# Optimization experiments

Measured on AMD Instinct MI355X. Metric: run time of the kernel, lower is better.

## Reference

```python
import jax, jax.numpy as jnp
import numpy as np

B = 131072      # batch
G = 8           # number of groups
GS = 8          # features per group (n_features = G*GS = 64)
K = 8           # n_basis
O = 16          # kan_out_dim
TOT = G * O     # 128, GroupKANLayer output dim
R = 10          # n_rules
FIN = 20        # fuzzy_in_dim = max(2*n_rules, 8)
EPS_BN = 1e-5


def setup_inputs() -> dict:
    key = jax.random.key(0)
    ks = jax.random.split(key, 8)
    x = jax.random.normal(ks[0], (B, G * GS), dtype=jnp.float32)
    # per-group GaussianRBF params (one shared RBF per group, applied to each feature)
    rbf_centres = jnp.tile(jnp.linspace(-3.0, 3.0, K, dtype=jnp.float32)[None, :], (G, 1))
    rbf_log_widths = jnp.zeros((G, K), dtype=jnp.float32)
    rbf_weights = jax.random.normal(ks[1], (G, K), dtype=jnp.float32) * 0.1
    rbf_linear_w = jnp.ones((G,), dtype=jnp.float32)
    # group projections: kaiming normal fan_in (relu gain sqrt(2))
    proj_W = jax.random.normal(ks[2], (G, O, GS), dtype=jnp.float32) * np.sqrt(2.0 / GS)
    proj_b = jnp.zeros((G, O), dtype=jnp.float32)
    bn1_gamma = jnp.ones((TOT,), dtype=jnp.float32)
    bn1_beta = jnp.zeros((TOT,), dtype=jnp.float32)
    # fuzzy_proj linear (xavier uniform) TOT -> FIN
    a = np.sqrt(6.0 / (TOT + FIN))
    fp_W = jax.random.uniform(ks[3], (FIN, TOT), dtype=jnp.float32, minval=-a, maxval=a)
    fp_b = jnp.zeros((FIN,), dtype=jnp.float32)
    bn2_gamma = jnp.ones((FIN,), dtype=jnp.float32)
    bn2_beta = jnp.zeros((FIN,), dtype=jnp.float32)
    # IT2 fuzzy layer params
    fz_centres = jax.random.uniform(ks[4], (R, FIN), dtype=jnp.float32, minval=-1.0, maxval=1.0)
    fz_log_su = jnp.full((R, FIN), -0.7, dtype=jnp.float32)
    fz_log_sl = jnp.full((R, FIN), -1.2, dtype=jnp.float32)
    # sparse rule head
    head_W = jax.random.normal(ks[5], (1, R), dtype=jnp.float32) * 0.05
    head_b = jnp.zeros((1,), dtype=jnp.float32)
    return {
        'x': x, 'rbf_centres': rbf_centres, 'rbf_log_widths': rbf_log_widths,
        'rbf_weights': rbf_weights, 'rbf_linear_w': rbf_linear_w,
        'proj_W': proj_W, 'proj_b': proj_b,
        'bn1_gamma': bn1_gamma, 'bn1_beta': bn1_beta,
        'fp_W': fp_W, 'fp_b': fp_b, 'bn2_gamma': bn2_gamma, 'bn2_beta': bn2_beta,
        'fz_centres': fz_centres, 'fz_log_su': fz_log_su, 'fz_log_sl': fz_log_sl,
        'head_W': head_W, 'head_b': head_b,
    }


def _batchnorm(h, gamma, beta):
    # training-mode BatchNorm1d: normalize with batch mean / biased variance
    mu = h.mean(axis=0)
    var = h.var(axis=0)
    return (h - mu) * jax.lax.rsqrt(var + EPS_BN) * gamma + beta


def _forward(x, rbf_centres, rbf_log_widths, rbf_weights, rbf_linear_w,
             proj_W, proj_b, bn1_gamma, bn1_beta, fp_W, fp_b,
             bn2_gamma, bn2_beta, fz_centres, fz_log_su, fz_log_sl,
             head_W, head_b):
    b = x.shape[0]
    xg = x.reshape(b, G, GS)                               # groups are contiguous index slices
    sigma = jnp.exp(rbf_log_widths) + 1e-6                 # [G,K]
    # Gaussian RBF over all groups/features at once: [B,G,GS,K]
    rbf = jnp.exp(-0.5 * ((xg[..., None] - rbf_centres[:, None, :]) / sigma[:, None, :]) ** 2)
    act = rbf_linear_w[None, :, None] * xg + jnp.einsum('bgfk,gk->bgf', rbf, rbf_weights)
    proj = jnp.einsum('bgf,gof->bgo', act, proj_W) + proj_b  # grouped linear, [B,G,O]
    h = _batchnorm(proj.reshape(b, TOT), bn1_gamma, bn1_beta)
    # fuzzy_proj: Linear -> BN -> GELU (torch default GELU = exact erf form)
    z = _batchnorm(h @ fp_W.T + fp_b, bn2_gamma, bn2_beta)
    z = jax.nn.gelu(z, approximate=False)                    # [B,FIN]
    # IT2 fuzzy memberships
    su = jnp.exp(fz_log_su) + 1e-6                           # [R,FIN]
    sl = jnp.minimum(jnp.exp(fz_log_sl) + 1e-6, su * 0.9)
    diff = z[:, None, :] - fz_centres[None]                  # [B,R,FIN]
    upper = jnp.exp(-0.5 * (diff / su[None]) ** 2).mean(-1)  # [B,R]
    lower = jnp.exp(-0.5 * (diff / sl[None]) ** 2).mean(-1)
    firing = 0.5 * (upper + lower)
    return firing @ head_W.T + head_b                        # [B,1]


def reference(x, rbf_centres, rbf_log_widths, rbf_weights, rbf_linear_w,
              proj_W, proj_b, bn1_gamma, bn1_beta, fp_W, fp_b,
              bn2_gamma, bn2_beta, fz_centres, fz_log_su, fz_log_sl,
              head_W, head_b):
    return _forward(x, rbf_centres, rbf_log_widths, rbf_weights, rbf_linear_w,
                    proj_W, proj_b, bn1_gamma, bn1_beta, fp_W, fp_b,
                    bn2_gamma, bn2_beta, fz_centres, fz_log_su, fz_log_sl,
                    head_W, head_b)
```

## Files before the change

### kernel.cpp

```cpp
#include <hip/hip_runtime.h>
#include <math.h>

#define B_N 131072
#define R_N 10
#define FIN_N 20

#define WS_STAT1 0
#define ST1_SZ   (64 * 352)
#define WS_MT    22528
#define WS_C     23808
#define WS_STAT2 23828
#define WS_NH    26388
#define WS_Z     26816

__global__ __launch_bounds__(256) void k_act_moments(
    const float* __restrict__ x, const float* __restrict__ cen,
    const float* __restrict__ lw, const float* __restrict__ rw,
    const float* __restrict__ linw, float* __restrict__ stat1)
{
    __shared__ float sAcc[4][8][44];

    const int t = threadIdx.x;
    const int g = t & 7;
    const int rl = t >> 3;

    float c_[8], nh_[8], w_[8];
#pragma unroll
    for (int k = 0; k < 8; ++k) {
        c_[k] = cen[g * 8 + k];
        float s = expf(lw[g * 8 + k]) + 1e-6f;
        nh_[k] = -0.5f / (s * s);
        w_[k] = rw[g * 8 + k];
    }
    const float lin = linw[g];

    float sumA[8], P[36];
#pragma unroll
    for (int f = 0; f < 8; ++f) sumA[f] = 0.0f;
#pragma unroll
    for (int i = 0; i < 36; ++i) P[i] = 0.0f;

    for (int row = blockIdx.x * 32 + rl; row < B_N; row += gridDim.x * 32) {
        const float* xr = x + (size_t)row * 64 + g * 8;
        float4 v0 = *(const float4*)(xr);
        float4 v1 = *(const float4*)(xr + 4);
        float xv[8] = {v0.x, v0.y, v0.z, v0.w, v1.x, v1.y, v1.z, v1.w};
        float act[8];
#pragma unroll
        for (int f = 0; f < 8; ++f) {
            float v = xv[f];
            float a = lin * v;
#pragma unroll
            for (int k = 0; k < 8; ++k) {
                float d = v - c_[k];
                a += w_[k] * __expf(d * d * nh_[k]);
            }
            act[f] = a;
        }
        int idx = 0;
#pragma unroll
        for (int f = 0; f < 8; ++f) {
            sumA[f] += act[f];
#pragma unroll
            for (int f2 = 0; f2 <= f; ++f2) { P[idx] += act[f] * act[f2]; ++idx; }
        }
    }

#pragma unroll
    for (int off = 32; off >= 8; off >>= 1) {
#pragma unroll
        for (int f = 0; f < 8; ++f) sumA[f] += __shfl_down(sumA[f], off, 64);
#pragma unroll
        for (int i = 0; i < 36; ++i) P[i] += __shfl_down(P[i], off, 64);
    }
    const int wave = t >> 6, lane = t & 63;
    if (lane < 8) {
        float* dst = &sAcc[wave][lane][0];
#pragma unroll
        for (int f = 0; f < 8; ++f) dst[f] = sumA[f];
#pragma unroll
        for (int i = 0; i < 36; ++i) dst[8 + i] = P[i];
    }
    __syncthreads();
    for (int i = t; i < 352; i += 256) {
        int gg = i / 44, v = i % 44;
        float s = sAcc[0][gg][v] + sAcc[1][gg][v] + sAcc[2][gg][v] + sAcc[3][gg][v];
        atomicAdd(&stat1[(blockIdx.x & 63) * 352 + i], s);
    }
}

__global__ __launch_bounds__(256) void k_build(
    const float* __restrict__ stat1, const float* __restrict__ fpW,
    const float* __restrict__ fpb, const float* __restrict__ g1,
    const float* __restrict__ b1, const float* __restrict__ Wp,
    const float* __restrict__ pb, const float* __restrict__ lsu,
    const float* __restrict__ lsl,
    float* __restrict__ Mt, float* __restrict__ Cc, float* __restrict__ nh,
    float* __restrict__ stat2)
{
    __shared__ float Am[8][8];
    __shared__ float Sg[8][36];
    __shared__ float a_[128], bb_[128];
    const int t = threadIdx.x;

    for (int i = t; i < 352; i += 256) {
        float s = 0.0f;
        for (int st = 0; st < 64; ++st) s += stat1[st * 352 + i];
        float m = s * (1.0f / B_N);
        int g = i / 44, v = i % 44;
        if (v < 8) Am[g][v] = m; else Sg[g][v - 8] = m;
    }
    __syncthreads();

    if (t < 128) {
        const int g = t >> 4;
        float wv[8];
#pragma unroll
        for (int f = 0; f < 8; ++f) wv[f] = Wp[t * 8 + f];
        float dot = 0.0f;
#pragma unroll
        for (int f = 0; f < 8; ++f) dot += wv[f] * Am[g][f];
        const float pbv = pb[t];
        const float mu = pbv + dot;
        float e2 = pbv * pbv + 2.0f * pbv * dot;
        int idx = 0;
#pragma unroll
        for (int f = 0; f < 8; ++f)
#pragma unroll
            for (int f2 = 0; f2 <= f; ++f2) {
                float c2 = (f2 == f) ? 1.0f : 2.0f;
                e2 += c2 * wv[f] * wv[f2] * Sg[g][idx]; ++idx;
            }
        const float var = e2 - mu * mu;
        const float a = g1[t] * rsqrtf(var + 1e-5f);
        a_[t] = a;
        bb_[t] = b1[t] - mu * a;
    }
    __syncthreads();

    for (int i = t; i < 1280; i += 256) {
        int gf = i / 20, j = i % 20;
        int g = gf >> 3, f = gf & 7;
        float m = 0.0f;
        for (int o = 0; o < 16; ++o) {
            int c = g * 16 + o;
            m += fpW[j * 128 + c] * a_[c] * Wp[c * 8 + f];
        }
        Mt[i] = m;
    }
    if (t < 20) {
        float cj = fpb[t];
        for (int c = 0; c < 128; ++c)
            cj += fpW[t * 128 + c] * (a_[c] * pb[c] + bb_[c]);
        Cc[t] = cj;
    }
    for (int i = t; i < 200; i += 256) {
        float su = expf(lsu[i]) + 1e-6f;
        float sl = fminf(expf(lsl[i]) + 1e-6f, 0.9f * su);
        nh[i] = -0.5f / (su * su);
        nh[200 + i] = -0.5f / (sl * sl);
    }
    for (int i = t; i < 2560; i += 256) stat2[i] = 0.0f;
}

__device__ __forceinline__ void zpre_row(
    const float* __restrict__ xr,
    const float4* __restrict__ sRbf,
    const float* __restrict__ sLin,
    const float* __restrict__ sMt,
    const float* __restrict__ sC,
    float zp[20])
{
#pragma unroll
    for (int j = 0; j < 20; ++j) zp[j] = sC[j];
#pragma unroll 1
    for (int g = 0; g < 8; ++g) {
        float4 v0 = *(const float4*)(xr + g * 8);
        float4 v1 = *(const float4*)(xr + g * 8 + 4);
        float xv[8] = {v0.x, v0.y, v0.z, v0.w, v1.x, v1.y, v1.z, v1.w};
        float act[8];
        float lin = sLin[g];
#pragma unroll
        for (int f = 0; f < 8; ++f) act[f] = lin * xv[f];
#pragma unroll 1
        for (int k = 0; k < 8; ++k) {
            float4 p = sRbf[g * 8 + k];
#pragma unroll
            for (int f = 0; f < 8; ++f) {
                float d = xv[f] - p.x;
                act[f] += p.y * __expf(d * d * p.z);
            }
        }
#pragma unroll 1
        for (int f = 0; f < 8; ++f) {
            float a = act[f];
            const float4* m4 = (const float4*)(sMt + (g * 8 + f) * 20);
            float4 ma = m4[0], mb = m4[1], mc = m4[2], md = m4[3], me = m4[4];
            zp[0] += a * ma.x; zp[1] += a * ma.y; zp[2] += a * ma.z; zp[3] += a * ma.w;
            zp[4] += a * mb.x; zp[5] += a * mb.y; zp[6] += a * mb.z; zp[7] += a * mb.w;
            zp[8] += a * mc.x; zp[9] += a * mc.y; zp[10] += a * mc.z; zp[11] += a * mc.w;
            zp[12] += a * md.x; zp[13] += a * md.y; zp[14] += a * md.z; zp[15] += a * md.w;
            zp[16] += a * me.x; zp[17] += a * me.y; zp[18] += a * me.z; zp[19] += a * me.w;
        }
    }
}

__device__ __forceinline__ void load_rbf_lds(
    const float* cen, const float* lw, const float* rw, const float* linw,
    const float* Mt, const float* Cc,
    float4* sRbf, float* sLin, float* sMt, float* sC, int t)
{
    if (t < 64) {
        float s = expf(lw[t]) + 1e-6f;
        sRbf[t] = make_float4(cen[t], rw[t], -0.5f / (s * s), 0.0f);
    }
    if (t < 8)  sLin[t] = linw[t];
    if (t < 20) sC[t] = Cc[t];
    for (int i = t; i < 1280; i += 256) sMt[i] = Mt[i];
}

__global__ __launch_bounds__(256) void k_zpre_stats(
    const float* __restrict__ x, const float* __restrict__ cen,
    const float* __restrict__ lw, const float* __restrict__ rw,
    const float* __restrict__ linw, const float* __restrict__ Mt,
    const float* __restrict__ Cc, float* __restrict__ zout,
    float* __restrict__ stat2, int store)
{
    __shared__ __align__(16) float4 sRbf[64];
    __shared__ float sLin[8], sC[20];
    __shared__ __align__(16) float sMt[1280];
    __shared__ float sRed[4][8][40];

    const int t = threadIdx.x;
    load_rbf_lds(cen, lw, rw, linw, Mt, Cc, sRbf, sLin, sMt, sC, t);
    __syncthreads();

    const int row = blockIdx.x * 256 + t;
    float zp[20];
    zpre_row(x + (size_t)row * 64, sRbf, sLin, sMt, sC, zp);

    if (store) {
#pragma unroll
        for (int j = 0; j < 20; ++j) zout[(size_t)j * B_N + row] = zp[j];
    }

    float s_[20], q_[20];
#pragma unroll
    for (int j = 0; j < 20; ++j) { s_[j] = zp[j]; q_[j] = zp[j] * zp[j]; }
#pragma unroll
    for (int off = 32; off >= 8; off >>= 1) {
#pragma unroll
        for (int j = 0; j < 20; ++j) {
            s_[j] += __shfl_down(s_[j], off, 64);
            q_[j] += __shfl_down(q_[j], off, 64);
        }
    }
    const int wave = t >> 6, lane = t & 63;
    if (lane < 8) {
#pragma unroll
        for (int j = 0; j < 20; ++j) {
            sRed[wave][lane][j] = s_[j];
            sRed[wave][lane][20 + j] = q_[j];
        }
    }
    __syncthreads();
    if (t < 40) {
        float v = 0.0f;
#pragma unroll
        for (int w = 0; w < 4; ++w)
#pragma unroll
            for (int l = 0; l < 8; ++l) v += sRed[w][l][t];
        atomicAdd(&stat2[(blockIdx.x & 63) * 40 + t], v);
    }
}

__device__ __forceinline__ float gelu_exact(float v) {
    return 0.5f * v * (1.0f + erff(v * 0.70710678118654752440f));
}

__device__ __forceinline__ float fuzzy_head(
    const float z[20], const float4* sFz, const float* sHW, float hb)
{
    float acc = hb;
#pragma unroll 1
    for (int r = 0; r < 10; ++r) {
        float u = 0.0f, l = 0.0f;
#pragma unroll
        for (int j = 0; j < 20; ++j) {
            float4 p = sFz[r * 20 + j];
            float d = z[j] - p.x;
            float dd = d * d;
            u += __expf(dd * p.y);
            l += __expf(dd * p.z);
        }
        acc += sHW[r] * 0.025f * (u + l);
    }
    return acc;
}

__device__ __forceinline__ void bn2_inline(
    const float* stat2, const float* g2, const float* b2,
    float* sT, float* sSc, float* sSh, int t)
{
    if (t < 40) {
        float s = 0.0f;
        for (int st = 0; st < 64; ++st) s += stat2[st * 40 + t];
        sT[t] = s;
    }
    __syncthreads();
    if (t < 20) {
        float mu = sT[t] * (1.0f / B_N);
        float var = sT[20 + t] * (1.0f / B_N) - mu * mu;
        float sc = g2[t] * rsqrtf(var + 1e-5f);
        sSc[t] = sc;
        sSh[t] = b2[t] - mu * sc;
    }
}

__global__ __launch_bounds__(256) void k_out_load(
    const float* __restrict__ zin, const float* __restrict__ stat2,
    const float* __restrict__ g2, const float* __restrict__ b2,
    const float* __restrict__ nh, const float* __restrict__ fzc,
    const float* __restrict__ hW, const float* __restrict__ hb,
    float* __restrict__ out)
{
    __shared__ float sT[40], sSc[20], sSh[20], sHW[10];
    __shared__ __align__(16) float4 sFz[200];
    const int t = threadIdx.x;
    if (t < 10) sHW[t] = hW[t];
    for (int i = t; i < 200; i += 256)
        sFz[i] = make_float4(fzc[i], nh[i], nh[200 + i], 0.0f);
    bn2_inline(stat2, g2, b2, sT, sSc, sSh, t);
    __syncthreads();

    const int row = blockIdx.x * 256 + t;
    float z[20];
#pragma unroll
    for (int j = 0; j < 20; ++j) {
        float zp = zin[(size_t)j * B_N + row];
        z[j] = gelu_exact(sSc[j] * zp + sSh[j]);
    }
    out[row] = fuzzy_head(z, sFz, sHW, hb[0]);
}

__global__ __launch_bounds__(256) void k_out_rec(
    const float* __restrict__ x, const float* __restrict__ cen,
    const float* __restrict__ lw, const float* __restrict__ rw,
    const float* __restrict__ linw, const float* __restrict__ Mt,
    const float* __restrict__ Cc, const float* __restrict__ stat2,
    const float* __restrict__ g2, const float* __restrict__ b2,
    const float* __restrict__ nh, const float* __restrict__ fzc,
    const float* __restrict__ hW, const float* __restrict__ hb,
    float* __restrict__ out)
{
    __shared__ __align__(16) float4 sRbf[64];
    __shared__ float sLin[8], sC[20];
    __shared__ __align__(16) float sMt[1280];
    __shared__ float sT[40], sSc[20], sSh[20], sHW[10];
    __shared__ __align__(16) float4 sFz[200];

    const int t = threadIdx.x;
    load_rbf_lds(cen, lw, rw, linw, Mt, Cc, sRbf, sLin, sMt, sC, t);
    if (t < 10) sHW[t] = hW[t];
    for (int i = t; i < 200; i += 256)
        sFz[i] = make_float4(fzc[i], nh[i], nh[200 + i], 0.0f);
    bn2_inline(stat2, g2, b2, sT, sSc, sSh, t);
    __syncthreads();

    const int row = blockIdx.x * 256 + t;
    float zp[20];
    zpre_row(x + (size_t)row * 64, sRbf, sLin, sMt, sC, zp);
    float z[20];
#pragma unroll
    for (int j = 0; j < 20; ++j)
        z[j] = gelu_exact(sSc[j] * zp[j] + sSh[j]);
    out[row] = fuzzy_head(z, sFz, sHW, hb[0]);
}

extern "C" void kernel_launch(void* const* d_in, const int* in_sizes, int n_in,
                              void* d_out, int out_size, void* d_ws, size_t ws_size,
                              hipStream_t stream) {
    const float* x    = (const float*)d_in[0];
    const float* cen  = (const float*)d_in[1];
    const float* lw   = (const float*)d_in[2];
    const float* rw   = (const float*)d_in[3];
    const float* linw = (const float*)d_in[4];
    const float* Wp   = (const float*)d_in[5];
    const float* pb   = (const float*)d_in[6];
    const float* g1   = (const float*)d_in[7];
    const float* b1   = (const float*)d_in[8];
    const float* fpW  = (const float*)d_in[9];
    const float* fpb  = (const float*)d_in[10];
    const float* g2   = (const float*)d_in[11];
    const float* b2   = (const float*)d_in[12];
    const float* fzc  = (const float*)d_in[13];
    const float* lsu  = (const float*)d_in[14];
    const float* lsl  = (const float*)d_in[15];
    const float* hW   = (const float*)d_in[16];
    const float* hb   = (const float*)d_in[17];

    float* ws    = (float*)d_ws;
    float* stat1 = ws + WS_STAT1;
    float* Mt    = ws + WS_MT;
    float* Cc    = ws + WS_C;
    float* stat2 = ws + WS_STAT2;
    float* nh    = ws + WS_NH;
    float* zbuf  = ws + WS_Z;
    float* outp  = (float*)d_out;

    const size_t need = ((size_t)WS_Z + (size_t)20 * B_N) * sizeof(float);
    const int store = (ws_size >= need) ? 1 : 0;

    hipMemsetAsync(stat1, 0, (size_t)ST1_SZ * sizeof(float), stream);
    k_act_moments<<<1024, 256, 0, stream>>>(x, cen, lw, rw, linw, stat1);
    k_build<<<1, 256, 0, stream>>>(stat1, fpW, fpb, g1, b1, Wp, pb, lsu, lsl,
                                   Mt, Cc, nh, stat2);
    k_zpre_stats<<<512, 256, 0, stream>>>(x, cen, lw, rw, linw, Mt, Cc,
                                          store ? zbuf : nullptr, stat2, store);
    if (store) {
        k_out_load<<<512, 256, 0, stream>>>(zbuf, stat2, g2, b2, nh, fzc, hW, hb, outp);
    } else {
        k_out_rec<<<512, 256, 0, stream>>>(x, cen, lw, rw, linw, Mt, Cc,
                                           stat2, g2, b2, nh, fzc, hW, hb, outp);
    }
}
```

Before: 182.3 us.

## Cache RBF activations to workspace and compute z from them with multi-row blocking

The first pass now writes the per-feature RBF activations (64 floats per row) to workspace when enough space exists. A new kernel then builds the pre-BN fuzzy inputs and their statistics from those cached activations, processing four rows per thread so each shared-memory matrix load is reused. This avoids recomputing the 64 exp calls per feature in the second pass. The output kernel now handles two rows per thread, and the warp reductions are shortened to a single lane per wave. The cost is an extra 32 MB write and read of activations, which only pays off if the workspace is large enough and the pass was compute bound.

```diff
diff --git a/kernel.cpp b/kernel.cpp
--- a/kernel.cpp
+++ b/kernel.cpp
@@ -9,14 +9,17 @@
 #define ST1_SZ   (64 * 352)
 #define WS_MT    22528
 #define WS_C     23808
-#define WS_STAT2 23828
-#define WS_NH    26388
-#define WS_Z     26816
+#define WS_STAT2 23840
+#define WS_NH    26400
+#define WS_ACT   26816
+#define WS_Z2    26816
+#define WS_ZFULL (26816 + (size_t)64 * B_N)
 
 __global__ __launch_bounds__(256) void k_act_moments(
     const float* __restrict__ x, const float* __restrict__ cen,
     const float* __restrict__ lw, const float* __restrict__ rw,
-    const float* __restrict__ linw, float* __restrict__ stat1)
+    const float* __restrict__ linw, float* __restrict__ act_out,
+    float* __restrict__ stat1, int store)
 {
     __shared__ float sAcc[4][8][44];
 
@@ -56,6 +59,11 @@
                 a += w_[k] * __expf(d * d * nh_[k]);
             }
             act[f] = a;
+        }
+        if (store) {
+            float* ar = act_out + (size_t)row * 64 + g * 8;
+            *(float4*)(ar)     = make_float4(act[0], act[1], act[2], act[3]);
+            *(float4*)(ar + 4) = make_float4(act[4], act[5], act[6], act[7]);
         }
         int idx = 0;
 #pragma unroll
@@ -163,13 +171,94 @@
     for (int i = t; i < 2560; i += 256) stat2[i] = 0.0f;
 }
 
+__global__ __launch_bounds__(128) void k_z_from_act(
+    const float* __restrict__ act, const float* __restrict__ Mt,
+    const float* __restrict__ Cc, float* __restrict__ zout,
+    float* __restrict__ stat2)
+{
+    __shared__ __align__(16) float sMt[1280];
+    __shared__ float sC[20];
+    __shared__ float sRed[2][40];
+
+    const int t = threadIdx.x;
+    for (int i = t; i < 1280; i += 128) sMt[i] = Mt[i];
+    if (t < 20) sC[t] = Cc[t];
+    __syncthreads();
+
+    const int r0 = (blockIdx.x * 128 + t) * 4;
+    float zp[4][20];
+#pragma unroll
+    for (int r = 0; r < 4; ++r)
+#pragma unroll
+        for (int j = 0; j < 20; ++j) zp[r][j] = sC[j];
+
+#pragma unroll 1
+    for (int g = 0; g < 8; ++g) {
+        float a[4][8];
+#pragma unroll
+        for (int r = 0; r < 4; ++r) {
+            const float* ar = act + (size_t)(r0 + r) * 64 + g * 8;
+            float4 v0 = *(const float4*)(ar);
+            float4 v1 = *(const float4*)(ar + 4);
+            a[r][0] = v0.x; a[r][1] = v0.y; a[r][2] = v0.z; a[r][3] = v0.w;
+            a[r][4] = v1.x; a[r][5] = v1.y; a[r][6] = v1.z; a[r][7] = v1.w;
+        }
+#pragma unroll
+        for (int f = 0; f < 8; ++f) {
+            const float4* m4 = (const float4*)(sMt + (g * 8 + f) * 20);
+            float4 ma = m4[0], mb = m4[1], mc = m4[2], md = m4[3], me = m4[4];
+#pragma unroll
+            for (int r = 0; r < 4; ++r) {
+                float av = a[r][f];
+                zp[r][0] += av * ma.x; zp[r][1] += av * ma.y; zp[r][2] += av * ma.z; zp[r][3] += av * ma.w;
+                zp[r][4] += av * mb.x; zp[r][5] += av * mb.y; zp[r][6] += av * mb.z; zp[r][7] += av * mb.w;
+                zp[r][8] += av * mc.x; zp[r][9] += av * mc.y; zp[r][10] += av * mc.z; zp[r][11] += av * mc.w;
+                zp[r][12] += av * md.x; zp[r][13] += av * md.y; zp[r][14] += av * md.z; zp[r][15] += av * md.w;
+                zp[r][16] += av * me.x; zp[r][17] += av * me.y; zp[r][18] += av * me.z; zp[r][19] += av * me.w;
+            }
+        }
+    }
+
+#pragma unroll
+    for (int j = 0; j < 20; ++j) {
+        *(float4*)(zout + (size_t)j * B_N + r0) =
+            make_float4(zp[0][j], zp[1][j], zp[2][j], zp[3][j]);
+    }
+
+    float s_[20], q_[20];
+#pragma unroll
+    for (int j = 0; j < 20; ++j) {
+        float s = zp[0][j] + zp[1][j] + zp[2][j] + zp[3][j];
+        float q = zp[0][j]*zp[0][j] + zp[1][j]*zp[1][j] + zp[2][j]*zp[2][j] + zp[3][j]*zp[3][j];
+        s_[j] = s; q_[j] = q;
+    }
+#pragma unroll
+    for (int off = 32; off >= 1; off >>= 1) {
+#pragma unroll
+        for (int j = 0; j < 20; ++j) {
+            s_[j] += __shfl_down(s_[j], off, 64);
+            q_[j] += __shfl_down(q_[j], off, 64);
+        }
+    }
+    const int wave = t >> 6, lane = t & 63;
+    if (lane == 0) {
+#pragma unroll
+        for (int j = 0; j < 20; ++j) {
+            sRed[wave][j] = s_[j];
+            sRed[wave][20 + j] = q_[j];
+        }
+    }
+    __syncthreads();
+    if (t < 40) {
+        float v = sRed[0][t] + sRed[1][t];
+        atomicAdd(&stat2[(blockIdx.x & 63) * 40 + t], v);
+    }
+}
+
 __device__ __forceinline__ void zpre_row(
-    const float* __restrict__ xr,
-    const float4* __restrict__ sRbf,
-    const float* __restrict__ sLin,
-    const float* __restrict__ sMt,
-    const float* __restrict__ sC,
-    float zp[20])
+    const float* __restrict__ xr, const float4* __restrict__ sRbf,
+    const float* __restrict__ sLin, const float* __restrict__ sMt,
+    const float* __restrict__ sC, float zp[20])
 {
 #pragma unroll
     for (int j = 0; j < 20; ++j) zp[j] = sC[j];
@@ -193,14 +282,14 @@
         }
 #pragma unroll 1
         for (int f = 0; f < 8; ++f) {
-            float a = act[f];
+            float av = act[f];
             const float4* m4 = (const float4*)(sMt + (g * 8 + f) * 20);
             float4 ma = m4[0], mb = m4[1], mc = m4[2], md = m4[3], me = m4[4];
-            zp[0] += a * ma.x; zp[1] += a * ma.y; zp[2] += a * ma.z; zp[3] += a * ma.w;
-            zp[4] += a * mb.x; zp[5] += a * mb.y; zp[6] += a * mb.z; zp[7] += a * mb.w;
-            zp[8] += a * mc.x; zp[9] += a * mc.y; zp[10] += a * mc.z; zp[11] += a * mc.w;
-            zp[12] += a * md.x; zp[13] += a * md.y; zp[14] += a * md.z; zp[15] += a * md.w;
-            zp[16] += a * me.x; zp[17] += a * me.y; zp[18] += a * me.z; zp[19] += a * me.w;
+            zp[0] += av * ma.x; zp[1] += av * ma.y; zp[2] += av * ma.z; zp[3] += av * ma.w;
+            zp[4] += av * mb.x; zp[5] += av * mb.y; zp[6] += av * mb.z; zp[7] += av * mb.w;
+            zp[8] += av * mc.x; zp[9] += av * mc.y; zp[10] += av * mc.z; zp[11] += av * mc.w;
+            zp[12] += av * md.x; zp[13] += av * md.y; zp[14] += av * md.z; zp[15] += av * md.w;
+            zp[16] += av * me.x; zp[17] += av * me.y; zp[18] += av * me.z; zp[19] += av * me.w;
         }
     }
 }
@@ -229,7 +318,7 @@
     __shared__ __align__(16) float4 sRbf[64];
     __shared__ float sLin[8], sC[20];
     __shared__ __align__(16) float sMt[1280];
-    __shared__ float sRed[4][8][40];
+    __shared__ float sRed[4][40];
 
     const int t = threadIdx.x;
     load_rbf_lds(cen, lw, rw, linw, Mt, Cc, sRbf, sLin, sMt, sC, t);
@@ -238,17 +327,15 @@
     const int row = blockIdx.x * 256 + t;
     float zp[20];
     zpre_row(x + (size_t)row * 64, sRbf, sLin, sMt, sC, zp);
-
     if (store) {
 #pragma unroll
         for (int j = 0; j < 20; ++j) zout[(size_t)j * B_N + row] = zp[j];
     }
-
     float s_[20], q_[20];
 #pragma unroll
     for (int j = 0; j < 20; ++j) { s_[j] = zp[j]; q_[j] = zp[j] * zp[j]; }
 #pragma unroll
-    for (int off = 32; off >= 8; off >>= 1) {
+    for (int off = 32; off >= 1; off >>= 1) {
 #pragma unroll
         for (int j = 0; j < 20; ++j) {
             s_[j] += __shfl_down(s_[j], off, 64);
@@ -256,46 +343,19 @@
         }
     }
     const int wave = t >> 6, lane = t & 63;
-    if (lane < 8) {
-#pragma unroll
-        for (int j = 0; j < 20; ++j) {
-            sRed[wave][lane][j] = s_[j];
-            sRed[wave][lane][20 + j] = q_[j];
-        }
+    if (lane == 0) {
+#pragma unroll
+        for (int j = 0; j < 20; ++j) { sRed[wave][j] = s_[j]; sRed[wave][20 + j] = q_[j]; }
     }
     __syncthreads();
     if (t < 40) {
-        float v = 0.0f;
-#pragma unroll
-        for (int w = 0; w < 4; ++w)
-#pragma unroll
-            for (int l = 0; l < 8; ++l) v += sRed[w][l][t];
+        float v = sRed[0][t] + sRed[1][t] + sRed[2][t] + sRed[3][t];
         atomicAdd(&stat2[(blockIdx.x & 63) * 40 + t], v);
     }
 }
 
 __device__ __forceinline__ float gelu_exact(float v) {
     return 0.5f * v * (1.0f + erff(v * 0.70710678118654752440f));
-}
-
-__device__ __forceinline__ float fuzzy_head(
-    const float z[20], const float4* sFz, const float* sHW, float hb)
-{
-    float acc = hb;
-#pragma unroll 1
-    for (int r = 0; r < 10; ++r) {
-        float u = 0.0f, l = 0.0f;
-#pragma unroll
-        for (int j = 0; j < 20; ++j) {
-            float4 p = sFz[r * 20 + j];
-            float d = z[j] - p.x;
-            float dd = d * d;
-            u += __expf(dd * p.y);
-            l += __expf(dd * p.z);
-        }
-        acc += sHW[r] * 0.025f * (u + l);
-    }
-    return acc;
 }
 
 __device__ __forceinline__ void bn2_inline(
@@ -317,7 +377,7 @@
     }
 }
 
-__global__ __launch_bounds__(256) void k_out_load(
+__global__ __launch_bounds__(256) void k_out2(
     const float* __restrict__ zin, const float* __restrict__ stat2,
     const float* __restrict__ g2, const float* __restrict__ b2,
     const float* __restrict__ nh, const float* __restrict__ fzc,
@@ -333,14 +393,32 @@
     bn2_inline(stat2, g2, b2, sT, sSc, sSh, t);
     __syncthreads();
 
-    const int row = blockIdx.x * 256 + t;
-    float z[20];
+    const int r0 = (blockIdx.x * 256 + t) * 2;
+    float z0[20], z1[20];
 #pragma unroll
     for (int j = 0; j < 20; ++j) {
-        float zp = zin[(size_t)j * B_N + row];
-        z[j] = gelu_exact(sSc[j] * zp + sSh[j]);
-    }
-    out[row] = fuzzy_head(z, sFz, sHW, hb[0]);
+        float2 v = *(const float2*)(zin + (size_t)j * B_N + r0);
+        z0[j] = gelu_exact(sSc[j] * v.x + sSh[j]);
+        z1[j] = gelu_exact(sSc[j] * v.y + sSh[j]);
+    }
+    const float hbv = hb[0];
+    float acc0 = hbv, acc1 = hbv;
+#pragma unroll 1
+    for (int r = 0; r < 10; ++r) {
+        float u0 = 0.0f, l0 = 0.0f, u1 = 0.0f, l1 = 0.0f;
+#pragma unroll
+        for (int j = 0; j < 20; ++j) {
+            float4 p = sFz[r * 20 + j];
+            float d0 = z0[j] - p.x, d1 = z1[j] - p.x;
+            float dd0 = d0 * d0, dd1 = d1 * d1;
+            u0 += __expf(dd0 * p.y); l0 += __expf(dd0 * p.z);
+            u1 += __expf(dd1 * p.y); l1 += __expf(dd1 * p.z);
+        }
+        float w = sHW[r] * 0.025f;
+        acc0 += w * (u0 + l0);
+        acc1 += w * (u1 + l1);
+    }
+    *(float2*)(out + r0) = make_float2(acc0, acc1);
 }
 
 __global__ __launch_bounds__(256) void k_out_rec(
@@ -374,7 +452,21 @@
 #pragma unroll
     for (int j = 0; j < 20; ++j)
         z[j] = gelu_exact(sSc[j] * zp[j] + sSh[j]);
-    out[row] = fuzzy_head(z, sFz, sHW, hb[0]);
+    float acc = hb[0];
+#pragma unroll 1
+    for (int r = 0; r < 10; ++r) {
+        float u = 0.0f, l = 0.0f;
+#pragma unroll
+        for (int j = 0; j < 20; ++j) {
+            float4 p = sFz[r * 20 + j];
+            float d = z[j] - p.x;
+            float dd = d * d;
+            u += __expf(dd * p.y);
+            l += __expf(dd * p.z);
+        }
+        acc += sHW[r] * 0.025f * (u + l);
+    }
+    out[row] = acc;
 }
 
 extern "C" void kernel_launch(void* const* d_in, const int* in_sizes, int n_in,
@@ -405,21 +497,29 @@
     float* Cc    = ws + WS_C;
     float* stat2 = ws + WS_STAT2;
     float* nh    = ws + WS_NH;
-    float* zbuf  = ws + WS_Z;
+    float* actb  = ws + WS_ACT;
     float* outp  = (float*)d_out;
 
-    const size_t need = ((size_t)WS_Z + (size_t)20 * B_N) * sizeof(float);
-    const int store = (ws_size >= need) ? 1 : 0;
+    const size_t needFull = (WS_ZFULL + (size_t)20 * B_N) * sizeof(float);
+    const size_t needZ    = ((size_t)WS_Z2 + (size_t)20 * B_N) * sizeof(float);
+    int mode = (ws_size >= needFull) ? 2 : (ws_size >= needZ ? 1 : 0);
+    float* zbuf = (mode == 2) ? (ws + WS_ZFULL) : (ws + WS_Z2);
 
     hipMemsetAsync(stat1, 0, (size_t)ST1_SZ * sizeof(float), stream);
-    k_act_moments<<<1024, 256, 0, stream>>>(x, cen, lw, rw, linw, stat1);
+    k_act_moments<<<1024, 256, 0, stream>>>(x, cen, lw, rw, linw, actb, stat1,
+                                            mode == 2 ? 1 : 0);
     k_build<<<1, 256, 0, stream>>>(stat1, fpW, fpb, g1, b1, Wp, pb, lsu, lsl,
                                    Mt, Cc, nh, stat2);
-    k_zpre_stats<<<512, 256, 0, stream>>>(x, cen, lw, rw, linw, Mt, Cc,
-                                          store ? zbuf : nullptr, stat2, store);
-    if (store) {
-        k_out_load<<<512, 256, 0, stream>>>(zbuf, stat2, g2, b2, nh, fzc, hW, hb, outp);
+    if (mode == 2) {
+        k_z_from_act<<<256, 128, 0, stream>>>(actb, Mt, Cc, zbuf, stat2);
+        k_out2<<<256, 256, 0, stream>>>(zbuf, stat2, g2, b2, nh, fzc, hW, hb, outp);
+    } else if (mode == 1) {
+        k_zpre_stats<<<512, 256, 0, stream>>>(x, cen, lw, rw, linw, Mt, Cc,
+                                              zbuf, stat2, 1);
+        k_out2<<<256, 256, 0, stream>>>(zbuf, stat2, g2, b2, nh, fzc, hW, hb, outp);
     } else {
+        k_zpre_stats<<<512, 256, 0, stream>>>(x, cen, lw, rw, linw, Mt, Cc,
+                                              nullptr, stat2, 0);
         k_out_rec<<<512, 256, 0, stream>>>(x, cen, lw, rw, linw, Mt, Cc,
                                            stat2, g2, b2, nh, fzc, hW, hb, outp);
     }
```

Result: slower. 188.5 us (+3.4%).
